# Kernel optimization log

Measured on AMD Instinct MI355X. Metric: run time of the kernel, lower is better.

Reference implementation:

```python
import jax, jax.numpy as jnp
import numpy as np

N_U, N_D = 64, 64
N_E = N_U + N_D
N_A = 32
N_SV, N_PV = 512, 64
# n1 = [4*N_A, N_SV, N_SV, N_SV]; n2 = [4, N_PV, N_PV, N_PV]


def setup_inputs() -> dict:
    key = jax.random.key(0)
    ks = jax.random.split(key, 32)
    n1 = [4 * N_A, N_SV, N_SV, N_SV]
    n2 = [4, N_PV, N_PV, N_PV]
    d = {}
    d['r'] = jax.random.normal(ks[0], (N_E, 3), jnp.float32)
    d['a'] = jax.random.normal(ks[1], (N_A, 3), jnp.float32)
    i = 2
    for l in range(3):
        fin = 3 * n1[l] + 2 * n2[l]
        d[f'V{l}_w'] = jax.random.normal(ks[i], (fin, n1[l + 1]), jnp.float32) / np.float32(np.sqrt(fin)); i += 1
        d[f'V{l}_b'] = jax.random.normal(ks[i], (n1[l + 1],), jnp.float32); i += 1
        d[f'W{l}_w'] = jax.random.normal(ks[i], (n2[l], n2[l + 1]), jnp.float32) / np.float32(np.sqrt(n2[l])); i += 1
        d[f'W{l}_b'] = jax.random.normal(ks[i], (n2[l + 1],), jnp.float32); i += 1
    fin = 3 * N_SV + 2 * N_PV
    d['after_w'] = jax.random.normal(ks[i], (fin, N_SV), jnp.float32) / np.float32(np.sqrt(fin)); i += 1
    d['after_b'] = jax.random.normal(ks[i], (N_SV,), jnp.float32); i += 1
    d['vhu_w'] = jax.random.normal(ks[i], (N_SV, N_SV // 2), jnp.float32) / np.float32(np.sqrt(N_SV)); i += 1
    d['vhu_b'] = jax.random.normal(ks[i], (N_SV // 2,), jnp.float32); i += 1
    d['vhd_w'] = jax.random.normal(ks[i], (N_SV, N_SV // 2), jnp.float32) / np.float32(np.sqrt(N_SV)); i += 1
    d['vhd_b'] = jax.random.normal(ks[i], (N_SV // 2,), jnp.float32); i += 1
    d['wu_w'] = jax.random.normal(ks[i], (N_SV // 2, N_U), jnp.float32) / np.float32(np.sqrt(N_SV // 2)); i += 1
    d['wu_b'] = jax.random.normal(ks[i], (N_U,), jnp.float32); i += 1
    d['wd_w'] = jax.random.normal(ks[i], (N_SV // 2, N_D), jnp.float32) / np.float32(np.sqrt(N_SV // 2)); i += 1
    d['wd_b'] = jax.random.normal(ks[i], (N_D,), jnp.float32); i += 1
    return d


def _fb_block(s_v, p_v):
    # s_v: (N_E, f_s), p_v: (N_E, N_E, f_p)
    s_u_mean = jnp.tile(s_v[:N_U].mean(0)[None, :], (N_E, 1))
    s_d_mean = jnp.tile(s_v[N_U:].mean(0)[None, :], (N_E, 1))
    p_u_mean = p_v[:N_U].mean(0)  # (N_E, f_p)
    p_d_mean = p_v[N_U:].mean(0)
    return jnp.concatenate([s_u_mean, s_d_mean, p_u_mean, p_d_mean, s_v], axis=-1)


def _forward(r, a, Vw, Vb, Ww, Wb, after_w, after_b, vhu_w, vhu_b, vhd_w, vhd_b, wu_w, wu_b, wd_w, wd_b):
    eye = jnp.eye(N_E, dtype=r.dtype)[:, :, None]
    ra = r[:, None, :] - a[None, :, :]                       # (N_E, N_A, 3)
    ra_len = jnp.linalg.norm(ra, axis=-1, keepdims=True)     # (N_E, N_A, 1)
    rr = r[None, :, :] - r[:, None, :]                       # (N_E, N_E, 3)
    rr_len = jnp.linalg.norm(rr + eye, axis=-1, keepdims=True) * (1.0 - eye)
    s_v = jnp.concatenate([ra, ra_len], axis=-1).reshape(N_E, -1)  # (N_E, 4*N_A)
    p_v = jnp.concatenate([rr, rr_len], axis=-1)                   # (N_E, N_E, 4)
    for vw, vb, ww, wb in zip(Vw, Vb, Ww, Wb):
        s_in = _fb_block(s_v, p_v)
        # NOTE: torch residual `s_v if s_v.shape[-1]==n_sv` never fires here:
        # fb_block output width is 3*n1+2*n2 != n_sv, so it adds zeros.
        s_v = jnp.tanh(s_in @ vw + vb)
        p_new = jnp.tanh(p_v @ ww + wb)
        p_v = p_new + (p_v if p_v.shape[-1] == N_PV else 0.0)
    s_in = _fb_block(s_v, p_v)
    s_v = jnp.tanh(s_in @ after_w + after_b)  # (N_E, N_SV); residual again never fires
    s_u = s_v[:N_U] @ vhu_w + vhu_b
    s_d = s_v[N_U:] @ vhd_w + vhd_b
    s_wu = s_u @ wu_w + wu_b   # (N_U, N_U)
    s_wd = s_d @ wd_w + wd_b   # (N_D, N_D)
    exp_u = jnp.linalg.norm(ra[:N_U], axis=-1, keepdims=True)  # (N_U, N_A, 1)
    exp_d = jnp.linalg.norm(ra[N_U:], axis=-1, keepdims=True)
    orb_u = (s_wu * jnp.exp(-exp_u).sum(axis=1))[None]  # (1, N_U, N_U)
    orb_d = (s_wd * jnp.exp(-exp_d).sum(axis=1))[None]
    # logabssumdet for two (1,n,n) matrices with n>1: no 1x1 dets.
    sgn_u, ld_u = jnp.linalg.slogdet(orb_u)
    sgn_d, ld_d = jnp.linalg.slogdet(orb_d)
    sign = sgn_u * sgn_d
    logdet = ld_u + ld_d        # (1,)
    maxlogdet = logdet.max()
    psi = (sign * jnp.exp(logdet - maxlogdet)).sum()
    return jnp.log(jnp.abs(psi)) + maxlogdet  # scalar log|psi|


def reference(r, a, V0_w, V0_b, V1_w, V1_b, V2_w, V2_b, W0_w, W0_b, W1_w, W1_b, W2_w, W2_b,
              after_w, after_b, vhu_w, vhu_b, vhd_w, vhd_b, wu_w, wu_b, wd_w, wd_b):
    Vw, Vb = [V0_w, V1_w, V2_w], [V0_b, V1_b, V2_b]
    Ww, Wb = [W0_w, W1_w, W2_w], [W0_b, W1_b, W2_b]
    return _forward(r, a, Vw, Vb, Ww, Wb, after_w, after_b,
                    vhu_w, vhu_b, vhd_w, vhd_b, wu_w, wu_b, wd_w, wd_b)
```

## Files before the change

kernel.cpp:

```cpp
#include <hip/hip_runtime.h>
#include <math.h>

#define NSV 512

__global__ __launch_bounds__(512)
void pchain_kernel(const float* __restrict__ r, const float* __restrict__ apos,
                   const float* __restrict__ W0w, const float* __restrict__ W0b,
                   const float* __restrict__ W1w, const float* __restrict__ W1b,
                   const float* __restrict__ W2w, const float* __restrict__ W2b,
                   float* __restrict__ sv0, float* __restrict__ expv,
                   float* __restrict__ pme0, float* __restrict__ pme1,
                   float* __restrict__ pme2, float* __restrict__ pme3)
{
    __shared__ float rL[384];
    __shared__ float W0l[256];
    __shared__ float shex[32];
    __shared__ __align__(16) float p0c[512];
    __shared__ __align__(16) float PA[128*68];
    __shared__ __align__(16) float Wbuf[4096];
    const int j = blockIdx.x;
    const int t = threadIdx.x;
    const int i  = t >> 2;
    const int oc = t & 3;
    const int o0 = oc * 16;

    if (t < 384) rL[t] = r[t];
    for (int idx = t; idx < 4096; idx += 512) Wbuf[idx] = W1w[idx];
    if (t < 256) W0l[t] = W0w[t];
    __syncthreads();

    const float rjx = rL[j*3+0], rjy = rL[j*3+1], rjz = rL[j*3+2];
    if (t < 128) {
        const int ii = t;
        float dx = rjx - rL[ii*3+0], dy = rjy - rL[ii*3+1], dz = rjz - rL[ii*3+2];
        float len = (ii == j) ? 0.f : sqrtf(dx*dx + dy*dy + dz*dz);
        p0c[ii*4+0]=dx; p0c[ii*4+1]=dy; p0c[ii*4+2]=dz; p0c[ii*4+3]=len;
    } else if (t < 160) {
        const int k = t - 128;
        float dx = rjx - apos[k*3+0], dy = rjy - apos[k*3+1], dz = rjz - apos[k*3+2];
        float len = sqrtf(dx*dx + dy*dy + dz*dz);
        float* sp = sv0 + (size_t)j*128 + k*4;
        sp[0]=dx; sp[1]=dy; sp[2]=dz; sp[3]=len;
        shex[k] = expf(-len);
    }
    __syncthreads();

    {
        const float x0=p0c[i*4+0], x1=p0c[i*4+1], x2=p0c[i*4+2], x3=p0c[i*4+3];
        #pragma unroll
        for (int k = 0; k < 16; ++k) {
            const int o = o0 + k;
            float acc = W0b[o];
            acc = fmaf(x0, W0l[o],     acc);
            acc = fmaf(x1, W0l[64+o],  acc);
            acc = fmaf(x2, W0l[128+o], acc);
            acc = fmaf(x3, W0l[192+o], acc);
            PA[i*68+o] = tanhf(acc);
        }
    }
    if (t < 8) {
        const int spin = t >> 2, c = t & 3;
        float s = 0.f;
        #pragma unroll 8
        for (int k = 0; k < 64; ++k) s += p0c[(spin*64+k)*4 + c];
        pme0[j*8 + t] = s * 0.015625f;
    }
    if (t == 8) {
        float s = 0.f;
        #pragma unroll 8
        for (int k = 0; k < 32; ++k) s += shex[k];
        expv[j] = s;
    }
    __syncthreads();

    if (t < 128) {
        const int spin = t >> 6, c = t & 63;
        float s = 0.f;
        #pragma unroll 8
        for (int k = 0; k < 64; ++k) s += PA[(spin*64+k)*68 + c];
        pme1[j*128 + t] = s * 0.015625f;
    }
    float acc[16], res[16];
    const float* pa = PA + i*68;
    {
        #pragma unroll
        for (int k = 0; k < 16; ++k) acc[k] = W1b[o0+k];
        #pragma unroll 4
        for (int c = 0; c < 64; ++c) {
            const float av = pa[c];
            const float* wr = Wbuf + c*64 + o0;
            float4 wa = *reinterpret_cast<const float4*>(wr);
            float4 wb = *reinterpret_cast<const float4*>(wr+4);
            float4 wc = *reinterpret_cast<const float4*>(wr+8);
            float4 wd = *reinterpret_cast<const float4*>(wr+12);
            acc[0] =fmaf(av,wa.x,acc[0]);  acc[1] =fmaf(av,wa.y,acc[1]);
            acc[2] =fmaf(av,wa.z,acc[2]);  acc[3] =fmaf(av,wa.w,acc[3]);
            acc[4] =fmaf(av,wb.x,acc[4]);  acc[5] =fmaf(av,wb.y,acc[5]);
            acc[6] =fmaf(av,wb.z,acc[6]);  acc[7] =fmaf(av,wb.w,acc[7]);
            acc[8] =fmaf(av,wc.x,acc[8]);  acc[9] =fmaf(av,wc.y,acc[9]);
            acc[10]=fmaf(av,wc.z,acc[10]); acc[11]=fmaf(av,wc.w,acc[11]);
            acc[12]=fmaf(av,wd.x,acc[12]); acc[13]=fmaf(av,wd.y,acc[13]);
            acc[14]=fmaf(av,wd.z,acc[14]); acc[15]=fmaf(av,wd.w,acc[15]);
        }
        #pragma unroll
        for (int k = 0; k < 16; ++k) res[k] = pa[o0+k];
    }
    __syncthreads();
    #pragma unroll
    for (int k = 0; k < 16; ++k) PA[i*68+o0+k] = tanhf(acc[k]) + res[k];
    __syncthreads();

    if (t < 128) {
        const int spin = t >> 6, c = t & 63;
        float s = 0.f;
        #pragma unroll 8
        for (int k = 0; k < 64; ++k) s += PA[(spin*64+k)*68 + c];
        pme2[j*128 + t] = s * 0.015625f;
    }
    for (int idx = t; idx < 4096; idx += 512) Wbuf[idx] = W2w[idx];
    __syncthreads();

    {
        #pragma unroll
        for (int k = 0; k < 16; ++k) acc[k] = W2b[o0+k];
        #pragma unroll 4
        for (int c = 0; c < 64; ++c) {
            const float av = pa[c];
            const float* wr = Wbuf + c*64 + o0;
            float4 wa = *reinterpret_cast<const float4*>(wr);
            float4 wb = *reinterpret_cast<const float4*>(wr+4);
            float4 wc = *reinterpret_cast<const float4*>(wr+8);
            float4 wd = *reinterpret_cast<const float4*>(wr+12);
            acc[0] =fmaf(av,wa.x,acc[0]);  acc[1] =fmaf(av,wa.y,acc[1]);
            acc[2] =fmaf(av,wa.z,acc[2]);  acc[3] =fmaf(av,wa.w,acc[3]);
            acc[4] =fmaf(av,wb.x,acc[4]);  acc[5] =fmaf(av,wb.y,acc[5]);
            acc[6] =fmaf(av,wb.z,acc[6]);  acc[7] =fmaf(av,wb.w,acc[7]);
            acc[8] =fmaf(av,wc.x,acc[8]);  acc[9] =fmaf(av,wc.y,acc[9]);
            acc[10]=fmaf(av,wc.z,acc[10]); acc[11]=fmaf(av,wc.w,acc[11]);
            acc[12]=fmaf(av,wd.x,acc[12]); acc[13]=fmaf(av,wd.y,acc[13]);
            acc[14]=fmaf(av,wd.z,acc[14]); acc[15]=fmaf(av,wd.w,acc[15]);
        }
        #pragma unroll
        for (int k = 0; k < 16; ++k) res[k] = pa[o0+k];
    }
    __syncthreads();
    #pragma unroll
    for (int k = 0; k < 16; ++k) PA[i*68+o0+k] = tanhf(acc[k]) + res[k];
    __syncthreads();

    if (t < 128) {
        const int spin = t >> 6, c = t & 63;
        float s = 0.f;
        #pragma unroll 8
        for (int k = 0; k < 64; ++k) s += PA[(spin*64+k)*68 + c];
        pme3[j*128 + t] = s * 0.015625f;
    }
}

template<int FS, int FP, bool L0>
__global__ __launch_bounds__(512)
void a2_kernel(const float* __restrict__ svIn, const float* __restrict__ pmeIn,
               const float* __restrict__ psumIn,
               const float* __restrict__ Vw, const float* __restrict__ Vb,
               float* __restrict__ svOut, float* __restrict__ psumOut)
{
    constexpr int KP  = 2*FP + FS;
    constexpr int KP2 = KP/2;
    __shared__ __align__(16) float As[4*KP];
    __shared__ __align__(16) float smL[2*FS];
    __shared__ __align__(16) float red[512];
    __shared__ float t1L[64];
    const int t  = threadIdx.x;
    const int et = blockIdx.x >> 3;
    const int e0 = et * 4;
    const int o0 = (blockIdx.x & 7) * 64;
    const int ol = t & 63;
    const int o  = o0 + ol;
    const int wv = t >> 6;

    for (int idx = t; idx < 4*2*FP; idx += 512)
        As[(idx/(2*FP))*KP + idx%(2*FP)] =
            pmeIn[(size_t)(e0 + idx/(2*FP))*(2*FP) + idx%(2*FP)];
    for (int idx = t; idx < FS; idx += 512) {
        const int row = idx / (FS/4), c4 = idx % (FS/4);
        *reinterpret_cast<float4*>(&As[row*KP + 2*FP + c4*4]) =
            *reinterpret_cast<const float4*>(&svIn[(size_t)(e0+row)*FS + c4*4]);
    }
    if (L0) {
        for (int idx = t; idx < 2*FS; idx += 512) {
            const int col = (idx < FS) ? idx : idx - FS;
            const int i0  = (idx < FS) ? 0 : 64;
            const float* base = svIn + (size_t)i0*FS + col;
            float s = 0.f;
            #pragma unroll 8
            for (int k = 0; k < 64; ++k) s += base[(size_t)k*FS];
            smL[idx] = s * 0.015625f;
        }
    } else {
        for (int idx = t; idx < 2*FS; idx += 512) {
            const int col = (idx < FS) ? idx : idx - FS;
            const int r0  = (idx < FS) ? 0 : 16;
            const float* base = psumIn + (size_t)r0*NSV + col;
            float s = 0.f;
            #pragma unroll
            for (int k = 0; k < 16; ++k) s += base[(size_t)k*NSV];
            smL[idx] = s * 0.015625f;
        }
    }
    __syncthreads();

    {
        constexpr int TI = (2*FS)/8;
        float a1 = 0.f;
        const float* Wp = Vw + (size_t)(wv*TI)*NSV + o;
        const float* mp = smL + wv*TI;
        #pragma unroll 8
        for (int k = 0; k < TI; ++k) a1 = fmaf(mp[k], Wp[(size_t)k*NSV], a1);
        red[wv*64 + ol] = a1;
    }
    __syncthreads();
    if (t < 64) {
        float s = Vb[o0 + t];
        #pragma unroll
        for (int g = 0; g < 8; ++g) s += red[g*64 + t];
        t1L[t] = s;
    }
    __syncthreads();

    const int e_l = wv & 3, kh = wv >> 2;
    {
        float a2 = (kh == 0) ? t1L[ol] : 0.f;
        const float* Ap = As + e_l*KP + kh*KP2;
        const float* Wp = Vw + (size_t)(2*FS + kh*KP2)*NSV + o;
        #pragma unroll 16
        for (int k = 0; k < KP2; ++k)
            a2 = fmaf(Ap[k], Wp[(size_t)k*NSV], a2);
        red[wv*64 + ol] = a2;
    }
    __syncthreads();
    float v = 0.f;
    if (t < 256) {
        v = tanhf(red[(t>>6)*64 + (t&63)] + red[((t>>6)+4)*64 + (t&63)]);
        svOut[(size_t)(e0 + (t>>6))*NSV + o0 + (t&63)] = v;
    }
    if (psumOut) {
        __syncthreads();
        if (t < 256) red[t] = v;
        __syncthreads();
        if (t < 64) {
            float s = red[t] + red[64+t] + red[128+t] + red[192+t];
            psumOut[(size_t)et*NSV + o0 + t] = s;
        }
    }
}

__global__ __launch_bounds__(512)
void headsw_kernel(const float* __restrict__ svF,
                   const float* __restrict__ vhu_w, const float* __restrict__ vhu_b,
                   const float* __restrict__ vhd_w, const float* __restrict__ vhd_b,
                   const float* __restrict__ wu_w,  const float* __restrict__ wu_b,
                   const float* __restrict__ wd_w,  const float* __restrict__ wd_b,
                   const float* __restrict__ expv,  float* __restrict__ orb)
{
    __shared__ __align__(16) float row[512];
    __shared__ __align__(16) float redH[512];
    __shared__ __align__(16) float tmpL[256];
    const int e = blockIdx.x;
    const int spin = e >> 6;
    const int t = threadIdx.x;
    row[t] = svF[(size_t)e*NSV + t];
    __syncthreads();

    const float* W1 = spin ? vhd_w : vhu_w;
    const float* B1 = spin ? vhd_b : vhu_b;
    {
        const int o = t & 255, kc = t >> 8;
        float acc = kc ? 0.f : B1[o];
        const float* Wp = W1 + (size_t)(kc*256)*256 + o;
        const float* rp = row + kc*256;
        #pragma unroll 8
        for (int f = 0; f < 256; ++f)
            acc = fmaf(rp[f], Wp[(size_t)f*256], acc);
        redH[t] = acc;
    }
    __syncthreads();
    if (t < 256) tmpL[t] = redH[t] + redH[256 + t];
    __syncthreads();

    const float* W2 = spin ? wd_w : wu_w;
    const float* B2 = spin ? wd_b : wu_b;
    {
        const int o = t & 63, kc = t >> 6;
        float acc = 0.f;
        const float* Wp = W2 + (size_t)(kc*32)*64 + o;
        const float* tp = tmpL + kc*32;
        #pragma unroll
        for (int f = 0; f < 32; ++f)
            acc = fmaf(tp[f], Wp[(size_t)f*64], acc);
        redH[kc*64 + o] = acc;
    }
    __syncthreads();
    if (t < 64) {
        float s = B2[t];
        #pragma unroll
        for (int g = 0; g < 8; ++g) s += redH[g*64 + t];
        orb[(size_t)e*64 + t] = s * expv[e];
    }
}

__device__ __forceinline__ int imax2(int a, int b) { return a > b ? a : b; }
__device__ __forceinline__ float readlane_f(float x, int lane) {
    return __int_as_float(__builtin_amdgcn_readlane(__float_as_int(x), lane));
}

__global__ __launch_bounds__(128)
void det_kernel(const float* __restrict__ orb, float* __restrict__ out)
{
    __shared__ float parts[2];
    const int t = threadIdx.x;
    const int w = t >> 6;
    const int lane = t & 63;
    const float* M = orb + (size_t)w*4096 + (size_t)lane*64;
    float rr[64];
    #pragma unroll
    for (int j = 0; j < 64; j += 4) {
        float4 v = *reinterpret_cast<const float4*>(M + j);
        rr[j]=v.x; rr[j+1]=v.y; rr[j+2]=v.z; rr[j+3]=v.w;
    }
    float pv_mine = 1.f;
    bool active = true;
    #pragma unroll
    for (int k = 0; k < 64; ++k) {
        int bits = (int)(__float_as_uint(rr[k]) & 0x7FFFFFC0u);
        int v = active ? (bits | lane) : lane;
        int tmp;
        tmp = __builtin_amdgcn_update_dpp(0, v, 0xB1,  0xF, 0xF, true); v = imax2(v, tmp);
        tmp = __builtin_amdgcn_update_dpp(0, v, 0x4E,  0xF, 0xF, true); v = imax2(v, tmp);
        tmp = __builtin_amdgcn_update_dpp(0, v, 0x141, 0xF, 0xF, true); v = imax2(v, tmp);
        tmp = __builtin_amdgcn_update_dpp(0, v, 0x140, 0xF, 0xF, true); v = imax2(v, tmp);
        tmp = __builtin_amdgcn_update_dpp(0, v, 0x142, 0xF, 0xF, true); v = imax2(v, tmp);
        tmp = __builtin_amdgcn_update_dpp(0, v, 0x143, 0xF, 0xF, true); v = imax2(v, tmp);
        const int idx = __builtin_amdgcn_readlane(v, 63) & 63;
        const float piv = readlane_f(rr[k], idx);
        pv_mine = (lane == k) ? piv : pv_mine;
        const float linv = __builtin_amdgcn_rcpf(piv);
        const float l = (active && lane != idx) ? rr[k]*linv : 0.f;
        if (lane == idx) active = false;
        #pragma unroll
        for (int j = k+1; j < 64; ++j)
            rr[j] = fmaf(-l, readlane_f(rr[j], idx), rr[j]);
    }
    float lg = logf(fabsf(pv_mine));
    #pragma unroll
    for (int off = 32; off; off >>= 1) lg += __shfl_down(lg, off);
    if (lane == 0) parts[w] = lg;
    __syncthreads();
    if (t == 0) out[0] = parts[0] + parts[1];
}

extern "C" void kernel_launch(void* const* d_in, const int* in_sizes, int n_in,
                              void* d_out, int out_size, void* d_ws, size_t ws_size,
                              hipStream_t stream)
{
    const float* r    = (const float*)d_in[0];
    const float* apos = (const float*)d_in[1];
    const float* V0w  = (const float*)d_in[2];
    const float* V0b  = (const float*)d_in[3];
    const float* W0w  = (const float*)d_in[4];
    const float* W0b  = (const float*)d_in[5];
    const float* V1w  = (const float*)d_in[6];
    const float* V1b  = (const float*)d_in[7];
    const float* W1w  = (const float*)d_in[8];
    const float* W1b  = (const float*)d_in[9];
    const float* V2w  = (const float*)d_in[10];
    const float* V2b  = (const float*)d_in[11];
    const float* W2w  = (const float*)d_in[12];
    const float* W2b  = (const float*)d_in[13];
    const float* afw  = (const float*)d_in[14];
    const float* afb  = (const float*)d_in[15];
    const float* vhuw = (const float*)d_in[16];
    const float* vhub = (const float*)d_in[17];
    const float* vhdw = (const float*)d_in[18];
    const float* vhdb = (const float*)d_in[19];
    const float* wuw  = (const float*)d_in[20];
    const float* wub  = (const float*)d_in[21];
    const float* wdw  = (const float*)d_in[22];
    const float* wdb  = (const float*)d_in[23];

    float* ws   = (float*)d_ws;
    float* sv0  = ws;
    float* svA  = sv0  + 16384;
    float* svB  = svA  + 65536;
    float* expv = svB  + 65536;
    float* pme0 = expv + 128;
    float* pme1 = pme0 + 1024;
    float* pme2 = pme1 + 16384;
    float* pme3 = pme2 + 16384;
    float* psA  = pme3 + 16384;
    float* psB  = psA  + 16384;
    float* orb  = psB  + 16384;

    pchain_kernel<<<128, 512, 0, stream>>>(r, apos, W0w, W0b, W1w, W1b, W2w, W2b,
                                           sv0, expv, pme0, pme1, pme2, pme3);
    a2_kernel<128, 4, true  ><<<256, 512, 0, stream>>>(sv0, pme0, nullptr, V0w, V0b, svA, psA);
    a2_kernel<512, 64, false><<<256, 512, 0, stream>>>(svA, pme1, psA, V1w, V1b, svB, psB);
    a2_kernel<512, 64, false><<<256, 512, 0, stream>>>(svB, pme2, psB, V2w, V2b, svA, psA);
    a2_kernel<512, 64, false><<<256, 512, 0, stream>>>(svA, pme3, psA, afw, afb, svB, nullptr);
    headsw_kernel<<<128, 512, 0, stream>>>(svB, vhuw, vhub, vhdw, vhdb,
                                           wuw, wub, wdw, wdb, expv, orb);
    det_kernel<<<1, 128, 0, stream>>>(orb, (float*)d_out);
}
```

Before: 98.25 us.

## Fuse seven kernel launches into one persistent kernel with global barriers

Merges the pchain, four a2 layers, heads and determinant kernels into a single 256-block persistent kernel that uses an atomic counter grid barrier between stages. Intermediate buffers are read and written through relaxed agent-scope atomic loads and stores so that data crosses blocks correctly. The aim is to remove the launch overhead and inter-kernel gaps of a short chain of small kernels. In exchange it relies on all 256 blocks being co-resident, spin-waits between stages, and gives up vectorized float4 loads on the sv input path.

```diff
diff --git a/kernel.cpp b/kernel.cpp
--- a/kernel.cpp
+++ b/kernel.cpp
@@ -3,26 +3,47 @@
 
 #define NSV 512
 
-__global__ __launch_bounds__(512)
-void pchain_kernel(const float* __restrict__ r, const float* __restrict__ apos,
-                   const float* __restrict__ W0w, const float* __restrict__ W0b,
-                   const float* __restrict__ W1w, const float* __restrict__ W1b,
-                   const float* __restrict__ W2w, const float* __restrict__ W2b,
-                   float* __restrict__ sv0, float* __restrict__ expv,
-                   float* __restrict__ pme0, float* __restrict__ pme1,
-                   float* __restrict__ pme2, float* __restrict__ pme3)
-{
-    __shared__ float rL[384];
-    __shared__ float W0l[256];
-    __shared__ float shex[32];
-    __shared__ __align__(16) float p0c[512];
-    __shared__ __align__(16) float PA[128*68];
-    __shared__ __align__(16) float Wbuf[4096];
-    const int j = blockIdx.x;
+__device__ unsigned g_bar  = 0;
+__device__ unsigned g_exit = 0;
+
+__device__ __forceinline__ float gload(const float* p) {
+    return __hip_atomic_load(p, __ATOMIC_RELAXED, __HIP_MEMORY_SCOPE_AGENT);
+}
+__device__ __forceinline__ void gstore(float* p, float v) {
+    __hip_atomic_store(p, v, __ATOMIC_RELAXED, __HIP_MEMORY_SCOPE_AGENT);
+}
+
+__device__ __forceinline__ void gsync(unsigned target) {
+    asm volatile("s_waitcnt vmcnt(0)" ::: "memory");
+    __syncthreads();
+    if (threadIdx.x == 0) {
+        atomicAdd(&g_bar, 1u);
+        while (__hip_atomic_load(&g_bar, __ATOMIC_RELAXED,
+                                 __HIP_MEMORY_SCOPE_AGENT) < target)
+            __builtin_amdgcn_s_sleep(4);
+    }
+    __syncthreads();
+}
+
+__device__ void pchain_role(int j, const float* __restrict__ r,
+                            const float* __restrict__ apos,
+                            const float* __restrict__ W0w, const float* __restrict__ W0b,
+                            const float* __restrict__ W1w, const float* __restrict__ W1b,
+                            const float* __restrict__ W2w, const float* __restrict__ W2b,
+                            float* __restrict__ sv0, float* __restrict__ expv,
+                            float* __restrict__ pme0, float* __restrict__ pme1,
+                            float* __restrict__ pme2, float* __restrict__ pme3,
+                            float* sh)
+{
+    float* rL   = sh;
+    float* W0l  = sh + 384;
+    float* shex = sh + 640;
+    float* p0c  = sh + 672;
+    float* PA   = sh + 1184;
+    float* Wbuf = sh + 9888;
     const int t = threadIdx.x;
     const int i  = t >> 2;
-    const int oc = t & 3;
-    const int o0 = oc * 16;
+    const int o0 = (t & 3) * 16;
 
     if (t < 384) rL[t] = r[t];
     for (int idx = t; idx < 4096; idx += 512) Wbuf[idx] = W1w[idx];
@@ -39,8 +60,10 @@
         const int k = t - 128;
         float dx = rjx - apos[k*3+0], dy = rjy - apos[k*3+1], dz = rjz - apos[k*3+2];
         float len = sqrtf(dx*dx + dy*dy + dz*dz);
-        float* sp = sv0 + (size_t)j*128 + k*4;
-        sp[0]=dx; sp[1]=dy; sp[2]=dz; sp[3]=len;
+        gstore(&sv0[(size_t)j*128 + k*4 + 0], dx);
+        gstore(&sv0[(size_t)j*128 + k*4 + 1], dy);
+        gstore(&sv0[(size_t)j*128 + k*4 + 2], dz);
+        gstore(&sv0[(size_t)j*128 + k*4 + 3], len);
         shex[k] = expf(-len);
     }
     __syncthreads();
@@ -63,13 +86,13 @@
         float s = 0.f;
         #pragma unroll 8
         for (int k = 0; k < 64; ++k) s += p0c[(spin*64+k)*4 + c];
-        pme0[j*8 + t] = s * 0.015625f;
+        gstore(&pme0[j*8 + t], s * 0.015625f);
     }
     if (t == 8) {
         float s = 0.f;
         #pragma unroll 8
         for (int k = 0; k < 32; ++k) s += shex[k];
-        expv[j] = s;
+        gstore(&expv[j], s);
     }
     __syncthreads();
 
@@ -78,7 +101,7 @@
         float s = 0.f;
         #pragma unroll 8
         for (int k = 0; k < 64; ++k) s += PA[(spin*64+k)*68 + c];
-        pme1[j*128 + t] = s * 0.015625f;
+        gstore(&pme1[j*128 + t], s * 0.015625f);
     }
     float acc[16], res[16];
     const float* pa = PA + i*68;
@@ -115,7 +138,7 @@
         float s = 0.f;
         #pragma unroll 8
         for (int k = 0; k < 64; ++k) s += PA[(spin*64+k)*68 + c];
-        pme2[j*128 + t] = s * 0.015625f;
+        gstore(&pme2[j*128 + t], s * 0.015625f);
     }
     for (int idx = t; idx < 4096; idx += 512) Wbuf[idx] = W2w[idx];
     __syncthreads();
@@ -153,57 +176,56 @@
         float s = 0.f;
         #pragma unroll 8
         for (int k = 0; k < 64; ++k) s += PA[(spin*64+k)*68 + c];
-        pme3[j*128 + t] = s * 0.015625f;
+        gstore(&pme3[j*128 + t], s * 0.015625f);
     }
 }
 
 template<int FS, int FP, bool L0>
-__global__ __launch_bounds__(512)
-void a2_kernel(const float* __restrict__ svIn, const float* __restrict__ pmeIn,
-               const float* __restrict__ psumIn,
-               const float* __restrict__ Vw, const float* __restrict__ Vb,
-               float* __restrict__ svOut, float* __restrict__ psumOut)
+__device__ void a2_role(int b, const float* __restrict__ svIn,
+                        const float* __restrict__ pmeIn,
+                        const float* __restrict__ psumIn,
+                        const float* __restrict__ Vw, const float* __restrict__ Vb,
+                        float* __restrict__ svOut, float* __restrict__ psumOut,
+                        float* sh)
 {
     constexpr int KP  = 2*FP + FS;
     constexpr int KP2 = KP/2;
-    __shared__ __align__(16) float As[4*KP];
-    __shared__ __align__(16) float smL[2*FS];
-    __shared__ __align__(16) float red[512];
-    __shared__ float t1L[64];
+    float* As  = sh;
+    float* smL = sh + 4*KP;
+    float* red = smL + 2*FS;
+    float* t1L = red + 512;
     const int t  = threadIdx.x;
-    const int et = blockIdx.x >> 3;
+    const int et = b >> 3;
     const int e0 = et * 4;
-    const int o0 = (blockIdx.x & 7) * 64;
+    const int o0 = (b & 7) * 64;
     const int ol = t & 63;
     const int o  = o0 + ol;
     const int wv = t >> 6;
 
     for (int idx = t; idx < 4*2*FP; idx += 512)
         As[(idx/(2*FP))*KP + idx%(2*FP)] =
-            pmeIn[(size_t)(e0 + idx/(2*FP))*(2*FP) + idx%(2*FP)];
-    for (int idx = t; idx < FS; idx += 512) {
-        const int row = idx / (FS/4), c4 = idx % (FS/4);
-        *reinterpret_cast<float4*>(&As[row*KP + 2*FP + c4*4]) =
-            *reinterpret_cast<const float4*>(&svIn[(size_t)(e0+row)*FS + c4*4]);
-    }
+            gload(&pmeIn[(size_t)(e0 + idx/(2*FP))*(2*FP) + idx%(2*FP)]);
+    for (int idx = t; idx < 4*FS; idx += 512)
+        As[(idx/FS)*KP + 2*FP + idx%FS] =
+            gload(&svIn[(size_t)(e0 + idx/FS)*FS + idx%FS]);
     if (L0) {
         for (int idx = t; idx < 2*FS; idx += 512) {
             const int col = (idx < FS) ? idx : idx - FS;
             const int i0  = (idx < FS) ? 0 : 64;
-            const float* base = svIn + (size_t)i0*FS + col;
             float s = 0.f;
             #pragma unroll 8
-            for (int k = 0; k < 64; ++k) s += base[(size_t)k*FS];
+            for (int k = 0; k < 64; ++k)
+                s += gload(&svIn[(size_t)(i0+k)*FS + col]);
             smL[idx] = s * 0.015625f;
         }
     } else {
         for (int idx = t; idx < 2*FS; idx += 512) {
             const int col = (idx < FS) ? idx : idx - FS;
             const int r0  = (idx < FS) ? 0 : 16;
-            const float* base = psumIn + (size_t)r0*NSV + col;
             float s = 0.f;
             #pragma unroll
-            for (int k = 0; k < 16; ++k) s += base[(size_t)k*NSV];
+            for (int k = 0; k < 16; ++k)
+                s += gload(&psumIn[(size_t)(r0+k)*NSV + col]);
             smL[idx] = s * 0.015625f;
         }
     }
@@ -241,7 +263,7 @@
     float v = 0.f;
     if (t < 256) {
         v = tanhf(red[(t>>6)*64 + (t&63)] + red[((t>>6)+4)*64 + (t&63)]);
-        svOut[(size_t)(e0 + (t>>6))*NSV + o0 + (t&63)] = v;
+        gstore(&svOut[(size_t)(e0 + (t>>6))*NSV + o0 + (t&63)], v);
     }
     if (psumOut) {
         __syncthreads();
@@ -249,26 +271,25 @@
         __syncthreads();
         if (t < 64) {
             float s = red[t] + red[64+t] + red[128+t] + red[192+t];
-            psumOut[(size_t)et*NSV + o0 + t] = s;
-        }
-    }
-}
-
-__global__ __launch_bounds__(512)
-void headsw_kernel(const float* __restrict__ svF,
-                   const float* __restrict__ vhu_w, const float* __restrict__ vhu_b,
-                   const float* __restrict__ vhd_w, const float* __restrict__ vhd_b,
-                   const float* __restrict__ wu_w,  const float* __restrict__ wu_b,
-                   const float* __restrict__ wd_w,  const float* __restrict__ wd_b,
-                   const float* __restrict__ expv,  float* __restrict__ orb)
-{
-    __shared__ __align__(16) float row[512];
-    __shared__ __align__(16) float redH[512];
-    __shared__ __align__(16) float tmpL[256];
-    const int e = blockIdx.x;
+            gstore(&psumOut[(size_t)et*NSV + o0 + t], s);
+        }
+    }
+}
+
+__device__ void headsw_role(int e, const float* __restrict__ svF,
+                            const float* __restrict__ vhu_w, const float* __restrict__ vhu_b,
+                            const float* __restrict__ vhd_w, const float* __restrict__ vhd_b,
+                            const float* __restrict__ wu_w,  const float* __restrict__ wu_b,
+                            const float* __restrict__ wd_w,  const float* __restrict__ wd_b,
+                            const float* __restrict__ expv,  float* __restrict__ orb,
+                            float* sh)
+{
+    float* row  = sh;
+    float* redH = sh + 512;
+    float* tmpL = sh + 1024;
     const int spin = e >> 6;
     const int t = threadIdx.x;
-    row[t] = svF[(size_t)e*NSV + t];
+    row[t] = gload(&svF[(size_t)e*NSV + t]);
     __syncthreads();
 
     const float* W1 = spin ? vhd_w : vhu_w;
@@ -304,7 +325,7 @@
         float s = B2[t];
         #pragma unroll
         for (int g = 0; g < 8; ++g) s += redH[g*64 + t];
-        orb[(size_t)e*64 + t] = s * expv[e];
+        gstore(&orb[(size_t)e*64 + t], s * gload(&expv[e]));
     }
 }
 
@@ -313,49 +334,112 @@
     return __int_as_float(__builtin_amdgcn_readlane(__float_as_int(x), lane));
 }
 
-__global__ __launch_bounds__(128)
-void det_kernel(const float* __restrict__ orb, float* __restrict__ out)
-{
-    __shared__ float parts[2];
+__device__ void det_role(const float* __restrict__ orb, float* __restrict__ out,
+                         float* sh)
+{
     const int t = threadIdx.x;
-    const int w = t >> 6;
-    const int lane = t & 63;
-    const float* M = orb + (size_t)w*4096 + (size_t)lane*64;
-    float rr[64];
-    #pragma unroll
-    for (int j = 0; j < 64; j += 4) {
-        float4 v = *reinterpret_cast<const float4*>(M + j);
-        rr[j]=v.x; rr[j+1]=v.y; rr[j+2]=v.z; rr[j+3]=v.w;
-    }
-    float pv_mine = 1.f;
-    bool active = true;
-    #pragma unroll
-    for (int k = 0; k < 64; ++k) {
-        int bits = (int)(__float_as_uint(rr[k]) & 0x7FFFFFC0u);
-        int v = active ? (bits | lane) : lane;
-        int tmp;
-        tmp = __builtin_amdgcn_update_dpp(0, v, 0xB1,  0xF, 0xF, true); v = imax2(v, tmp);
-        tmp = __builtin_amdgcn_update_dpp(0, v, 0x4E,  0xF, 0xF, true); v = imax2(v, tmp);
-        tmp = __builtin_amdgcn_update_dpp(0, v, 0x141, 0xF, 0xF, true); v = imax2(v, tmp);
-        tmp = __builtin_amdgcn_update_dpp(0, v, 0x140, 0xF, 0xF, true); v = imax2(v, tmp);
-        tmp = __builtin_amdgcn_update_dpp(0, v, 0x142, 0xF, 0xF, true); v = imax2(v, tmp);
-        tmp = __builtin_amdgcn_update_dpp(0, v, 0x143, 0xF, 0xF, true); v = imax2(v, tmp);
-        const int idx = __builtin_amdgcn_readlane(v, 63) & 63;
-        const float piv = readlane_f(rr[k], idx);
-        pv_mine = (lane == k) ? piv : pv_mine;
-        const float linv = __builtin_amdgcn_rcpf(piv);
-        const float l = (active && lane != idx) ? rr[k]*linv : 0.f;
-        if (lane == idx) active = false;
-        #pragma unroll
-        for (int j = k+1; j < 64; ++j)
-            rr[j] = fmaf(-l, readlane_f(rr[j], idx), rr[j]);
-    }
-    float lg = logf(fabsf(pv_mine));
-    #pragma unroll
-    for (int off = 32; off; off >>= 1) lg += __shfl_down(lg, off);
-    if (lane == 0) parts[w] = lg;
-    __syncthreads();
-    if (t == 0) out[0] = parts[0] + parts[1];
+    if (t < 128) {
+        const int w = t >> 6;
+        const int lane = t & 63;
+        const float* M = orb + (size_t)w*4096 + (size_t)lane*64;
+        float rr[64];
+        #pragma unroll
+        for (int j = 0; j < 64; ++j) rr[j] = gload(M + j);
+        float pv_mine = 1.f;
+        bool active = true;
+        #pragma unroll
+        for (int k = 0; k < 64; ++k) {
+            int bits = (int)(__float_as_uint(rr[k]) & 0x7FFFFFC0u);
+            int v = active ? (bits | lane) : lane;
+            int tmp;
+            tmp = __builtin_amdgcn_update_dpp(0, v, 0xB1,  0xF, 0xF, true); v = imax2(v, tmp);
+            tmp = __builtin_amdgcn_update_dpp(0, v, 0x4E,  0xF, 0xF, true); v = imax2(v, tmp);
+            tmp = __builtin_amdgcn_update_dpp(0, v, 0x141, 0xF, 0xF, true); v = imax2(v, tmp);
+            tmp = __builtin_amdgcn_update_dpp(0, v, 0x140, 0xF, 0xF, true); v = imax2(v, tmp);
+            tmp = __builtin_amdgcn_update_dpp(0, v, 0x142, 0xF, 0xF, true); v = imax2(v, tmp);
+            tmp = __builtin_amdgcn_update_dpp(0, v, 0x143, 0xF, 0xF, true); v = imax2(v, tmp);
+            const int idx = __builtin_amdgcn_readlane(v, 63) & 63;
+            const float piv = readlane_f(rr[k], idx);
+            pv_mine = (lane == k) ? piv : pv_mine;
+            const float linv = __builtin_amdgcn_rcpf(piv);
+            const float l = (active && lane != idx) ? rr[k]*linv : 0.f;
+            if (lane == idx) active = false;
+            #pragma unroll
+            for (int j = k+1; j < 64; ++j)
+                rr[j] = fmaf(-l, readlane_f(rr[j], idx), rr[j]);
+        }
+        float lg = logf(fabsf(pv_mine));
+        #pragma unroll
+        for (int off = 32; off; off >>= 1) lg += __shfl_down(lg, off);
+        if (lane == 0) sh[w] = lg;
+    }
+    __syncthreads();
+    if (t == 0) gstore(&out[0], sh[0] + sh[1]);
+}
+
+__global__ void __launch_bounds__(512)
+fused_ansatz(const float* __restrict__ r,    const float* __restrict__ apos,
+             const float* __restrict__ V0w,  const float* __restrict__ V0b,
+             const float* __restrict__ W0w,  const float* __restrict__ W0b,
+             const float* __restrict__ V1w,  const float* __restrict__ V1b,
+             const float* __restrict__ W1w,  const float* __restrict__ W1b,
+             const float* __restrict__ V2w,  const float* __restrict__ V2b,
+             const float* __restrict__ W2w,  const float* __restrict__ W2b,
+             const float* __restrict__ afw,  const float* __restrict__ afb,
+             const float* __restrict__ vhuw, const float* __restrict__ vhub,
+             const float* __restrict__ vhdw, const float* __restrict__ vhdb,
+             const float* __restrict__ wuw,  const float* __restrict__ wub,
+             const float* __restrict__ wdw,  const float* __restrict__ wdb,
+             float* __restrict__ ws, float* __restrict__ out)
+{
+    __shared__ __align__(16) float sh[13984];
+    const int b = blockIdx.x;
+    const int t = threadIdx.x;
+
+    float* sv0  = ws;
+    float* svA  = sv0  + 16384;
+    float* svB  = svA  + 65536;
+    float* expv = svB  + 65536;
+    float* pme0 = expv + 128;
+    float* pme1 = pme0 + 1024;
+    float* pme2 = pme1 + 16384;
+    float* pme3 = pme2 + 16384;
+    float* psA  = pme3 + 16384;
+    float* psB  = psA  + 16384;
+    float* orb  = psB  + 16384;
+
+    if (b < 128)
+        pchain_role(b, r, apos, W0w, W0b, W1w, W1b, W2w, W2b,
+                    sv0, expv, pme0, pme1, pme2, pme3, sh);
+    gsync(256);
+
+    a2_role<128, 4, true  >(b, sv0, pme0, nullptr, V0w, V0b, svA, psA, sh);
+    gsync(512);
+    a2_role<512, 64, false>(b, svA, pme1, psA, V1w, V1b, svB, psB, sh);
+    gsync(768);
+    a2_role<512, 64, false>(b, svB, pme2, psB, V2w, V2b, svA, psA, sh);
+    gsync(1024);
+    a2_role<512, 64, false>(b, svA, pme3, psA, afw, afb, svB, nullptr, sh);
+    gsync(1280);
+
+    if (b < 128)
+        headsw_role(b, svB, vhuw, vhub, vhdw, vhdb, wuw, wub, wdw, wdb,
+                    expv, orb, sh);
+    gsync(1536);
+
+    if (b == 0) det_role(orb, out, sh);
+
+    __syncthreads();
+    if (t == 0) {
+        atomicAdd(&g_exit, 1u);
+        if (b == 0) {
+            while (__hip_atomic_load(&g_exit, __ATOMIC_RELAXED,
+                                     __HIP_MEMORY_SCOPE_AGENT) < 256u)
+                __builtin_amdgcn_s_sleep(4);
+            atomicExch(&g_bar,  0u);
+            atomicExch(&g_exit, 0u);
+        }
+    }
 }
 
 extern "C" void kernel_launch(void* const* d_in, const int* in_sizes, int n_in,
@@ -387,26 +471,8 @@
     const float* wdw  = (const float*)d_in[22];
     const float* wdb  = (const float*)d_in[23];
 
-    float* ws   = (float*)d_ws;
-    float* sv0  = ws;
-    float* svA  = sv0  + 16384;
-    float* svB  = svA  + 65536;
-    float* expv = svB  + 65536;
-    float* pme0 = expv + 128;
-    float* pme1 = pme0 + 1024;
-    float* pme2 = pme1 + 16384;
-    float* pme3 = pme2 + 16384;
-    float* psA  = pme3 + 16384;
-    float* psB  = psA  + 16384;
-    float* orb  = psB  + 16384;
-
-    pchain_kernel<<<128, 512, 0, stream>>>(r, apos, W0w, W0b, W1w, W1b, W2w, W2b,
-                                           sv0, expv, pme0, pme1, pme2, pme3);
-    a2_kernel<128, 4, true  ><<<256, 512, 0, stream>>>(sv0, pme0, nullptr, V0w, V0b, svA, psA);
-    a2_kernel<512, 64, false><<<256, 512, 0, stream>>>(svA, pme1, psA, V1w, V1b, svB, psB);
-    a2_kernel<512, 64, false><<<256, 512, 0, stream>>>(svB, pme2, psB, V2w, V2b, svA, psA);
-    a2_kernel<512, 64, false><<<256, 512, 0, stream>>>(svA, pme3, psA, afw, afb, svB, nullptr);
-    headsw_kernel<<<128, 512, 0, stream>>>(svB, vhuw, vhub, vhdw, vhdb,
-                                           wuw, wub, wdw, wdb, expv, orb);
-    det_kernel<<<1, 128, 0, stream>>>(orb, (float*)d_out);
-}
+    fused_ansatz<<<dim3(256), dim3(512), 0, stream>>>(
+        r, apos, V0w, V0b, W0w, W0b, V1w, V1b, W1w, W1b,
+        V2w, V2b, W2w, W2b, afw, afb, vhuw, vhub, vhdw, vhdb,
+        wuw, wub, wdw, wdb, (float*)d_ws, (float*)d_out);
+}
```

Measured after the change: 136.9 us. +39.4%, slower.

## Fuse layer-0 V projection into front pair-chain kernel, dropping a launch

Applied to the files above, without the earlier changes.

Folds the first layer's single-stream linear (V0) into the pair-chain kernel. Each block now recomputes the per-spin single-stream means over electron-atom features locally and does a 392-input matvec for its own electron row. This removes one kernel launch and the sv0/pme0 round trips through global memory. In exchange, every block redundantly recomputes the spin means and reads all of V0w per electron. The layer-1 a2 kernel now computes its column sums directly from svA.

```diff
diff --git a/kernel.cpp b/kernel.cpp
--- a/kernel.cpp
+++ b/kernel.cpp
@@ -4,27 +4,35 @@
 #define NSV 512
 
 __global__ __launch_bounds__(512)
-void pchain_kernel(const float* __restrict__ r, const float* __restrict__ apos,
-                   const float* __restrict__ W0w, const float* __restrict__ W0b,
-                   const float* __restrict__ W1w, const float* __restrict__ W1b,
-                   const float* __restrict__ W2w, const float* __restrict__ W2b,
-                   float* __restrict__ sv0, float* __restrict__ expv,
-                   float* __restrict__ pme0, float* __restrict__ pme1,
-                   float* __restrict__ pme2, float* __restrict__ pme3)
+void front_kernel(const float* __restrict__ r,   const float* __restrict__ apos,
+                  const float* __restrict__ V0w, const float* __restrict__ V0b,
+                  const float* __restrict__ W0w, const float* __restrict__ W0b,
+                  const float* __restrict__ W1w, const float* __restrict__ W1b,
+                  const float* __restrict__ W2w, const float* __restrict__ W2b,
+                  float* __restrict__ svA,  float* __restrict__ expv,
+                  float* __restrict__ pme1, float* __restrict__ pme2,
+                  float* __restrict__ pme3)
 {
-    __shared__ float rL[384];
-    __shared__ float W0l[256];
-    __shared__ float shex[32];
-    __shared__ __align__(16) float p0c[512];
-    __shared__ __align__(16) float PA[128*68];
-    __shared__ __align__(16) float Wbuf[4096];
+    __shared__ __align__(16) float sh[14984];
+    float* rL    = sh;
+    float* W0l   = sh + 384;
+    float* svj   = sh + 640;
+    float* shex  = sh + 768;
+    float* pme0j = sh + 800;
+    float* aposL = sh + 808;
+    float* sm0   = sh + 904;
+    float* p0c   = sh + 1160;
+    float* PA    = sh + 1672;
+    float* Wbuf  = sh + 10376;
+    float* t1L   = sh + 14472;
+
     const int j = blockIdx.x;
     const int t = threadIdx.x;
     const int i  = t >> 2;
-    const int oc = t & 3;
-    const int o0 = oc * 16;
+    const int o0 = (t & 3) * 16;
 
     if (t < 384) rL[t] = r[t];
+    if (t < 96)  aposL[t] = apos[t];
     for (int idx = t; idx < 4096; idx += 512) Wbuf[idx] = W1w[idx];
     if (t < 256) W0l[t] = W0w[t];
     __syncthreads();
@@ -37,10 +45,9 @@
         p0c[ii*4+0]=dx; p0c[ii*4+1]=dy; p0c[ii*4+2]=dz; p0c[ii*4+3]=len;
     } else if (t < 160) {
         const int k = t - 128;
-        float dx = rjx - apos[k*3+0], dy = rjy - apos[k*3+1], dz = rjz - apos[k*3+2];
+        float dx = rjx - aposL[k*3+0], dy = rjy - aposL[k*3+1], dz = rjz - aposL[k*3+2];
         float len = sqrtf(dx*dx + dy*dy + dz*dz);
-        float* sp = sv0 + (size_t)j*128 + k*4;
-        sp[0]=dx; sp[1]=dy; sp[2]=dz; sp[3]=len;
+        svj[k*4+0]=dx; svj[k*4+1]=dy; svj[k*4+2]=dz; svj[k*4+3]=len;
         shex[k] = expf(-len);
     }
     __syncthreads();
@@ -63,7 +70,7 @@
         float s = 0.f;
         #pragma unroll 8
         for (int k = 0; k < 64; ++k) s += p0c[(spin*64+k)*4 + c];
-        pme0[j*8 + t] = s * 0.015625f;
+        pme0j[t] = s * 0.015625f;
     }
     if (t == 8) {
         float s = 0.f;
@@ -155,9 +162,42 @@
         for (int k = 0; k < 64; ++k) s += PA[(spin*64+k)*68 + c];
         pme3[j*128 + t] = s * 0.015625f;
     }
-}
-
-template<int FS, int FP, bool L0>
+
+    {
+        const int out = t >> 1, half = t & 1;
+        const int spin = out >> 7, cc = out & 127, a_i = cc >> 2, d = cc & 3;
+        const float ax = aposL[a_i*3+0], ay = aposL[a_i*3+1], az = aposL[a_i*3+2];
+        float s = 0.f;
+        #pragma unroll 8
+        for (int q = 0; q < 32; ++q) {
+            const int e = spin*64 + half*32 + q;
+            float dx = rL[e*3+0]-ax, dy = rL[e*3+1]-ay, dz = rL[e*3+2]-az;
+            float len = sqrtf(dx*dx + dy*dy + dz*dz);
+            s += (d==0)?dx:(d==1)?dy:(d==2)?dz:len;
+        }
+        t1L[t] = s;
+    }
+    __syncthreads();
+    if (t < 256) sm0[t] = (t1L[2*t] + t1L[2*t+1]) * 0.015625f;
+    __syncthreads();
+
+    {
+        const int o = t;
+        float a0 = V0b[o];
+        #pragma unroll 8
+        for (int c = 0; c < 256; ++c)
+            a0 = fmaf(sm0[c], V0w[(size_t)c*NSV + o], a0);
+        #pragma unroll
+        for (int c = 0; c < 8; ++c)
+            a0 = fmaf(pme0j[c], V0w[(size_t)(256+c)*NSV + o], a0);
+        #pragma unroll 8
+        for (int f = 0; f < 128; ++f)
+            a0 = fmaf(svj[f], V0w[(size_t)(264+f)*NSV + o], a0);
+        svA[(size_t)j*NSV + o] = tanhf(a0);
+    }
+}
+
+template<int FS, int FP, bool COLSUM>
 __global__ __launch_bounds__(512)
 void a2_kernel(const float* __restrict__ svIn, const float* __restrict__ pmeIn,
                const float* __restrict__ psumIn,
@@ -186,7 +226,7 @@
         *reinterpret_cast<float4*>(&As[row*KP + 2*FP + c4*4]) =
             *reinterpret_cast<const float4*>(&svIn[(size_t)(e0+row)*FS + c4*4]);
     }
-    if (L0) {
+    if (COLSUM) {
         for (int idx = t; idx < 2*FS; idx += 512) {
             const int col = (idx < FS) ? idx : idx - FS;
             const int i0  = (idx < FS) ? 0 : 64;
@@ -388,22 +428,20 @@
     const float* wdb  = (const float*)d_in[23];
 
     float* ws   = (float*)d_ws;
-    float* sv0  = ws;
-    float* svA  = sv0  + 16384;
+    float* svA  = ws;
     float* svB  = svA  + 65536;
     float* expv = svB  + 65536;
-    float* pme0 = expv + 128;
-    float* pme1 = pme0 + 1024;
+    float* pme1 = expv + 128;
     float* pme2 = pme1 + 16384;
     float* pme3 = pme2 + 16384;
     float* psA  = pme3 + 16384;
     float* psB  = psA  + 16384;
     float* orb  = psB  + 16384;
 
-    pchain_kernel<<<128, 512, 0, stream>>>(r, apos, W0w, W0b, W1w, W1b, W2w, W2b,
-                                           sv0, expv, pme0, pme1, pme2, pme3);
-    a2_kernel<128, 4, true  ><<<256, 512, 0, stream>>>(sv0, pme0, nullptr, V0w, V0b, svA, psA);
-    a2_kernel<512, 64, false><<<256, 512, 0, stream>>>(svA, pme1, psA, V1w, V1b, svB, psB);
+    front_kernel<<<128, 512, 0, stream>>>(r, apos, V0w, V0b, W0w, W0b,
+                                          W1w, W1b, W2w, W2b,
+                                          svA, expv, pme1, pme2, pme3);
+    a2_kernel<512, 64, true ><<<256, 512, 0, stream>>>(svA, pme1, nullptr, V1w, V1b, svB, psB);
     a2_kernel<512, 64, false><<<256, 512, 0, stream>>>(svB, pme2, psB, V2w, V2b, svA, psA);
     a2_kernel<512, 64, false><<<256, 512, 0, stream>>>(svA, pme3, psA, afw, afb, svB, nullptr);
     headsw_kernel<<<128, 512, 0, stream>>>(svB, vhuw, vhub, vhdw, vhdb,
```

After: 132.7 us. 35.0% more time.

## Split pairwise chain across spin halves and recompute layer-0 spin means in-kernel

Applied to the files above, without the earlier changes.

The pairwise-feature chain kernel now launches two blocks per electron, each handling one spin half of partner electrons with 8 outputs per thread instead of 16. This doubles parallelism and reduces per-thread register pressure. The layer-0 a2 kernel now recomputes the electron-atom spin means directly from positions instead of strided global reads of sv0, which removes a dependency on scattered loads. The cost is that W1/W2 weights are loaded twice as often across blocks and every layer-0 block does some redundant geometry work.

```diff
diff --git a/kernel.cpp b/kernel.cpp
--- a/kernel.cpp
+++ b/kernel.cpp
@@ -12,35 +12,38 @@
                    float* __restrict__ pme0, float* __restrict__ pme1,
                    float* __restrict__ pme2, float* __restrict__ pme3)
 {
-    __shared__ float rL[384];
-    __shared__ float W0l[256];
-    __shared__ float shex[32];
-    __shared__ __align__(16) float p0c[512];
-    __shared__ __align__(16) float PA[128*68];
-    __shared__ __align__(16) float Wbuf[4096];
-    const int j = blockIdx.x;
-    const int t = threadIdx.x;
-    const int i  = t >> 2;
-    const int oc = t & 3;
-    const int o0 = oc * 16;
+    __shared__ __align__(16) float sh[9472];
+    float* rL    = sh;
+    float* W0l   = sh + 384;
+    float* aposL = sh + 640;
+    float* shex  = sh + 736;
+    float* p0c   = sh + 768;
+    float* PA    = sh + 1024;
+    float* Wbuf  = sh + 5376;
+    const int b  = blockIdx.x;
+    const int j  = b >> 1, sp = b & 1;
+    const int t  = threadIdx.x;
+    const int i  = t >> 3;
+    const int o0 = (t & 7) * 8;
 
     if (t < 384) rL[t] = r[t];
+    else if (t < 480) aposL[t - 384] = apos[t - 384];
     for (int idx = t; idx < 4096; idx += 512) Wbuf[idx] = W1w[idx];
     if (t < 256) W0l[t] = W0w[t];
     __syncthreads();
 
     const float rjx = rL[j*3+0], rjy = rL[j*3+1], rjz = rL[j*3+2];
-    if (t < 128) {
-        const int ii = t;
+    if (t < 64) {
+        const int ii = sp*64 + t;
         float dx = rjx - rL[ii*3+0], dy = rjy - rL[ii*3+1], dz = rjz - rL[ii*3+2];
         float len = (ii == j) ? 0.f : sqrtf(dx*dx + dy*dy + dz*dz);
-        p0c[ii*4+0]=dx; p0c[ii*4+1]=dy; p0c[ii*4+2]=dz; p0c[ii*4+3]=len;
-    } else if (t < 160) {
-        const int k = t - 128;
-        float dx = rjx - apos[k*3+0], dy = rjy - apos[k*3+1], dz = rjz - apos[k*3+2];
+        p0c[t*4+0]=dx; p0c[t*4+1]=dy; p0c[t*4+2]=dz; p0c[t*4+3]=len;
+    } else if (sp == 0 && t < 96) {
+        const int k = t - 64;
+        float dx = rjx - aposL[k*3+0], dy = rjy - aposL[k*3+1], dz = rjz - aposL[k*3+2];
         float len = sqrtf(dx*dx + dy*dy + dz*dz);
-        float* sp = sv0 + (size_t)j*128 + k*4;
-        sp[0]=dx; sp[1]=dy; sp[2]=dz; sp[3]=len;
+        float* spp = sv0 + (size_t)j*128 + k*4;
+        spp[0]=dx; spp[1]=dy; spp[2]=dz; spp[3]=len;
         shex[k] = expf(-len);
     }
     __syncthreads();
@@ -48,24 +51,23 @@
     {
         const float x0=p0c[i*4+0], x1=p0c[i*4+1], x2=p0c[i*4+2], x3=p0c[i*4+3];
         #pragma unroll
-        for (int k = 0; k < 16; ++k) {
+        for (int k = 0; k < 8; ++k) {
             const int o = o0 + k;
-            float acc = W0b[o];
-            acc = fmaf(x0, W0l[o],     acc);
-            acc = fmaf(x1, W0l[64+o],  acc);
-            acc = fmaf(x2, W0l[128+o], acc);
-            acc = fmaf(x3, W0l[192+o], acc);
-            PA[i*68+o] = tanhf(acc);
-        }
-    }
-    if (t < 8) {
-        const int spin = t >> 2, c = t & 3;
+            float a = W0b[o];
+            a = fmaf(x0, W0l[o],     a);
+            a = fmaf(x1, W0l[64+o],  a);
+            a = fmaf(x2, W0l[128+o], a);
+            a = fmaf(x3, W0l[192+o], a);
+            PA[i*68+o] = tanhf(a);
+        }
+    }
+    if (t < 4) {
         float s = 0.f;
         #pragma unroll 8
-        for (int k = 0; k < 64; ++k) s += p0c[(spin*64+k)*4 + c];
-        pme0[j*8 + t] = s * 0.015625f;
-    }
-    if (t == 8) {
+        for (int k = 0; k < 64; ++k) s += p0c[k*4 + t];
+        pme0[j*8 + sp*4 + t] = s * 0.015625f;
+    }
+    if (sp == 0 && t == 4) {
         float s = 0.f;
         #pragma unroll 8
         for (int k = 0; k < 32; ++k) s += shex[k];
@@ -73,94 +75,80 @@
     }
     __syncthreads();
 
-    if (t < 128) {
-        const int spin = t >> 6, c = t & 63;
+    if (t < 64) {
         float s = 0.f;
         #pragma unroll 8
-        for (int k = 0; k < 64; ++k) s += PA[(spin*64+k)*68 + c];
-        pme1[j*128 + t] = s * 0.015625f;
-    }
-    float acc[16], res[16];
+        for (int k = 0; k < 64; ++k) s += PA[k*68 + t];
+        pme1[j*128 + sp*64 + t] = s * 0.015625f;
+    }
+    float acc[8], res[8];
     const float* pa = PA + i*68;
     {
         #pragma unroll
-        for (int k = 0; k < 16; ++k) acc[k] = W1b[o0+k];
+        for (int k = 0; k < 8; ++k) acc[k] = W1b[o0+k];
         #pragma unroll 4
         for (int c = 0; c < 64; ++c) {
             const float av = pa[c];
             const float* wr = Wbuf + c*64 + o0;
             float4 wa = *reinterpret_cast<const float4*>(wr);
             float4 wb = *reinterpret_cast<const float4*>(wr+4);
-            float4 wc = *reinterpret_cast<const float4*>(wr+8);
-            float4 wd = *reinterpret_cast<const float4*>(wr+12);
-            acc[0] =fmaf(av,wa.x,acc[0]);  acc[1] =fmaf(av,wa.y,acc[1]);
-            acc[2] =fmaf(av,wa.z,acc[2]);  acc[3] =fmaf(av,wa.w,acc[3]);
-            acc[4] =fmaf(av,wb.x,acc[4]);  acc[5] =fmaf(av,wb.y,acc[5]);
-            acc[6] =fmaf(av,wb.z,acc[6]);  acc[7] =fmaf(av,wb.w,acc[7]);
-            acc[8] =fmaf(av,wc.x,acc[8]);  acc[9] =fmaf(av,wc.y,acc[9]);
-            acc[10]=fmaf(av,wc.z,acc[10]); acc[11]=fmaf(av,wc.w,acc[11]);
-            acc[12]=fmaf(av,wd.x,acc[12]); acc[13]=fmaf(av,wd.y,acc[13]);
-            acc[14]=fmaf(av,wd.z,acc[14]); acc[15]=fmaf(av,wd.w,acc[15]);
-        }
-        #pragma unroll
-        for (int k = 0; k < 16; ++k) res[k] = pa[o0+k];
+            acc[0]=fmaf(av,wa.x,acc[0]); acc[1]=fmaf(av,wa.y,acc[1]);
+            acc[2]=fmaf(av,wa.z,acc[2]); acc[3]=fmaf(av,wa.w,acc[3]);
+            acc[4]=fmaf(av,wb.x,acc[4]); acc[5]=fmaf(av,wb.y,acc[5]);
+            acc[6]=fmaf(av,wb.z,acc[6]); acc[7]=fmaf(av,wb.w,acc[7]);
+        }
+        #pragma unroll
+        for (int k = 0; k < 8; ++k) res[k] = pa[o0+k];
     }
     __syncthreads();
     #pragma unroll
-    for (int k = 0; k < 16; ++k) PA[i*68+o0+k] = tanhf(acc[k]) + res[k];
-    __syncthreads();
-
-    if (t < 128) {
-        const int spin = t >> 6, c = t & 63;
+    for (int k = 0; k < 8; ++k) PA[i*68+o0+k] = tanhf(acc[k]) + res[k];
+    __syncthreads();
+
+    if (t < 64) {
         float s = 0.f;
         #pragma unroll 8
-        for (int k = 0; k < 64; ++k) s += PA[(spin*64+k)*68 + c];
-        pme2[j*128 + t] = s * 0.015625f;
+        for (int k = 0; k < 64; ++k) s += PA[k*68 + t];
+        pme2[j*128 + sp*64 + t] = s * 0.015625f;
     }
     for (int idx = t; idx < 4096; idx += 512) Wbuf[idx] = W2w[idx];
     __syncthreads();
 
     {
         #pragma unroll
-        for (int k = 0; k < 16; ++k) acc[k] = W2b[o0+k];
+        for (int k = 0; k < 8; ++k) acc[k] = W2b[o0+k];
         #pragma unroll 4
         for (int c = 0; c < 64; ++c) {
             const float av = pa[c];
             const float* wr = Wbuf + c*64 + o0;
             float4 wa = *reinterpret_cast<const float4*>(wr);
             float4 wb = *reinterpret_cast<const float4*>(wr+4);
-            float4 wc = *reinterpret_cast<const float4*>(wr+8);
-            float4 wd = *reinterpret_cast<const float4*>(wr+12);
-            acc[0] =fmaf(av,wa.x,acc[0]);  acc[1] =fmaf(av,wa.y,acc[1]);
-            acc[2] =fmaf(av,wa.z,acc[2]);  acc[3] =fmaf(av,wa.w,acc[3]);
-            acc[4] =fmaf(av,wb.x,acc[4]);  acc[5] =fmaf(av,wb.y,acc[5]);
-            acc[6] =fmaf(av,wb.z,acc[6]);  acc[7] =fmaf(av,wb.w,acc[7]);
-            acc[8] =fmaf(av,wc.x,acc[8]);  acc[9] =fmaf(av,wc.y,acc[9]);
-            acc[10]=fmaf(av,wc.z,acc[10]); acc[11]=fmaf(av,wc.w,acc[11]);
-            acc[12]=fmaf(av,wd.x,acc[12]); acc[13]=fmaf(av,wd.y,acc[13]);
-            acc[14]=fmaf(av,wd.z,acc[14]); acc[15]=fmaf(av,wd.w,acc[15]);
-        }
-        #pragma unroll
-        for (int k = 0; k < 16; ++k) res[k] = pa[o0+k];
+            acc[0]=fmaf(av,wa.x,acc[0]); acc[1]=fmaf(av,wa.y,acc[1]);
+            acc[2]=fmaf(av,wa.z,acc[2]); acc[3]=fmaf(av,wa.w,acc[3]);
+            acc[4]=fmaf(av,wb.x,acc[4]); acc[5]=fmaf(av,wb.y,acc[5]);
+            acc[6]=fmaf(av,wb.z,acc[6]); acc[7]=fmaf(av,wb.w,acc[7]);
+        }
+        #pragma unroll
+        for (int k = 0; k < 8; ++k) res[k] = pa[o0+k];
     }
     __syncthreads();
     #pragma unroll
-    for (int k = 0; k < 16; ++k) PA[i*68+o0+k] = tanhf(acc[k]) + res[k];
-    __syncthreads();
-
-    if (t < 128) {
-        const int spin = t >> 6, c = t & 63;
+    for (int k = 0; k < 8; ++k) PA[i*68+o0+k] = tanhf(acc[k]) + res[k];
+    __syncthreads();
+
+    if (t < 64) {
         float s = 0.f;
         #pragma unroll 8
-        for (int k = 0; k < 64; ++k) s += PA[(spin*64+k)*68 + c];
-        pme3[j*128 + t] = s * 0.015625f;
-    }
-}
-
-template<int FS, int FP, bool L0>
+        for (int k = 0; k < 64; ++k) s += PA[k*68 + t];
+        pme3[j*128 + sp*64 + t] = s * 0.015625f;
+    }
+}
+
+template<int FS, int FP, bool GEOM>
 __global__ __launch_bounds__(512)
 void a2_kernel(const float* __restrict__ svIn, const float* __restrict__ pmeIn,
                const float* __restrict__ psumIn,
+               const float* __restrict__ r, const float* __restrict__ apos,
                const float* __restrict__ Vw, const float* __restrict__ Vb,
                float* __restrict__ svOut, float* __restrict__ psumOut)
 {
@@ -170,6 +158,8 @@
     __shared__ __align__(16) float smL[2*FS];
     __shared__ __align__(16) float red[512];
     __shared__ float t1L[64];
+    __shared__ float rL[384];
+    __shared__ float aposL[96];
     const int t  = threadIdx.x;
     const int et = blockIdx.x >> 3;
     const int e0 = et * 4;
@@ -186,16 +176,26 @@
         *reinterpret_cast<float4*>(&As[row*KP + 2*FP + c4*4]) =
             *reinterpret_cast<const float4*>(&svIn[(size_t)(e0+row)*FS + c4*4]);
     }
-    if (L0) {
-        for (int idx = t; idx < 2*FS; idx += 512) {
-            const int col = (idx < FS) ? idx : idx - FS;
-            const int i0  = (idx < FS) ? 0 : 64;
-            const float* base = svIn + (size_t)i0*FS + col;
+    if (GEOM) {
+        if (t < 384) rL[t] = r[t];
+        else if (t < 480) aposL[t - 384] = apos[t - 384];
+        __syncthreads();
+        {
+            const int out = t >> 1, half = t & 1;
+            const int spin = out >> 7, cc = out & 127, a_i = cc >> 2, d = cc & 3;
+            const float ax = aposL[a_i*3+0], ay = aposL[a_i*3+1], az = aposL[a_i*3+2];
             float s = 0.f;
             #pragma unroll 8
-            for (int k = 0; k < 64; ++k) s += base[(size_t)k*FS];
-            smL[idx] = s * 0.015625f;
-        }
+            for (int q = 0; q < 32; ++q) {
+                const int e = spin*64 + half*32 + q;
+                float dx = rL[e*3+0]-ax, dy = rL[e*3+1]-ay, dz = rL[e*3+2]-az;
+                float len = sqrtf(dx*dx + dy*dy + dz*dz);
+                s += (d==0)?dx:(d==1)?dy:(d==2)?dz:len;
+            }
+            red[t] = s;
+        }
+        __syncthreads();
+        if (t < 256) smL[t] = (red[2*t] + red[2*t+1]) * 0.015625f;
     } else {
         for (int idx = t; idx < 2*FS; idx += 512) {
             const int col = (idx < FS) ? idx : idx - FS;
@@ -400,12 +400,16 @@
     float* psB  = psA  + 16384;
     float* orb  = psB  + 16384;
 
-    pchain_kernel<<<128, 512, 0, stream>>>(r, apos, W0w, W0b, W1w, W1b, W2w, W2b,
+    pchain_kernel<<<256, 512, 0, stream>>>(r, apos, W0w, W0b, W1w, W1b, W2w, W2b,
                                            sv0, expv, pme0, pme1, pme2, pme3);
-    a2_kernel<128, 4, true  ><<<256, 512, 0, stream>>>(sv0, pme0, nullptr, V0w, V0b, svA, psA);
-    a2_kernel<512, 64, false><<<256, 512, 0, stream>>>(svA, pme1, psA, V1w, V1b, svB, psB);
-    a2_kernel<512, 64, false><<<256, 512, 0, stream>>>(svB, pme2, psB, V2w, V2b, svA, psA);
-    a2_kernel<512, 64, false><<<256, 512, 0, stream>>>(svA, pme3, psA, afw, afb, svB, nullptr);
+    a2_kernel<128, 4, true  ><<<256, 512, 0, stream>>>(sv0, pme0, nullptr, r, apos,
+                                                       V0w, V0b, svA, psA);
+    a2_kernel<512, 64, false><<<256, 512, 0, stream>>>(svA, pme1, psA, r, apos,
+                                                       V1w, V1b, svB, psB);
+    a2_kernel<512, 64, false><<<256, 512, 0, stream>>>(svB, pme2, psB, r, apos,
+                                                       V2w, V2b, svA, psA);
+    a2_kernel<512, 64, false><<<256, 512, 0, stream>>>(svA, pme3, psA, r, apos,
+                                                       afw, afb, svB, nullptr);
     headsw_kernel<<<128, 512, 0, stream>>>(svB, vhuw, vhub, vhdw, vhdb,
                                            wuw, wub, wdw, wdb, expv, orb);
     det_kernel<<<1, 128, 0, stream>>>(orb, (float*)d_out);
```

Measured after the change: 105.5 us. +7.3%, slower.
